# Kernel optimization log

Hardware: AMD Instinct MI355X
Metric: run time of the kernel (lower is better)

The kernel has to match this reference:

```python
import jax, jax.numpy as jnp
import numpy as np

DIM = 512
NL = 4
P = 8
B = 4
L = 8192  # byte-level sequence length
LP = L // P  # patch-level sequence length


def _ln(x, g, b, eps=1e-5):
    m = jnp.mean(x, axis=-1, keepdims=True)
    v = jnp.mean((x - m) ** 2, axis=-1, keepdims=True)
    return (x - m) * jax.lax.rsqrt(v + eps) * g + b


def setup_inputs() -> dict:
    key = jax.random.key(0)
    ks = jax.random.split(key, 24)
    s = 0.02
    inp = {
        "bytes_in": jax.random.randint(ks[0], (B, L), 0, 256, dtype=jnp.int32),
        "byte_emb": jax.random.normal(ks[1], (256, DIM), jnp.float32) * s,
        # patch encoder Conv1d(kernel=stride=P): weight laid out [P, D_in, D_out]
        "enc_w": jax.random.normal(ks[2], (P, DIM, DIM), jnp.float32) * s,
        "enc_b": jnp.zeros((DIM,), jnp.float32),
        "hash_proj": jax.random.normal(ks[3], (DIM, DIM), jnp.float32) * s,
        # per-layer stacked params
        "qkv_w": jax.random.normal(ks[4], (NL, DIM, 3 * DIM), jnp.float32) * s,
        "qkv_b": jnp.zeros((NL, 3 * DIM), jnp.float32),
        "gate_w": jax.random.normal(ks[5], (NL, DIM, DIM), jnp.float32) * s,
        "gate_b": jnp.zeros((NL, DIM), jnp.float32),
        "ln1_g": jnp.ones((NL, DIM), jnp.float32),
        "ln1_b": jnp.zeros((NL, DIM), jnp.float32),
        "mlp_w1": jax.random.normal(ks[6], (NL, DIM, 4 * DIM), jnp.float32) * s,
        "mlp_b1": jnp.zeros((NL, 4 * DIM), jnp.float32),
        "mlp_w2": jax.random.normal(ks[7], (NL, 4 * DIM, DIM), jnp.float32) * s,
        "mlp_b2": jnp.zeros((NL, DIM), jnp.float32),
        "ln2_g": jnp.ones((NL, DIM), jnp.float32),
        "ln2_b": jnp.zeros((NL, DIM), jnp.float32),
        # patch decoder ConvTranspose1d(kernel=stride=P): weight [D_in, P, D_out]
        "dec_w": jax.random.normal(ks[8], (DIM, P, DIM), jnp.float32) * s,
        "dec_b": jnp.zeros((DIM,), jnp.float32),
        "head_w": jax.random.normal(ks[9], (DIM, 256), jnp.float32) * s,
        "head_b": jnp.zeros((256,), jnp.float32),
    }
    return inp


def reference(bytes_in, byte_emb, enc_w, enc_b, hash_proj,
              qkv_w, qkv_b, gate_w, gate_b, ln1_g, ln1_b,
              mlp_w1, mlp_b1, mlp_w2, mlp_b2, ln2_g, ln2_b,
              dec_w, dec_b, head_w, head_b):
    # byte embedding: [B, L, D]
    x = byte_emb[bytes_in]
    # non-overlapping Conv1d(kernel=stride=P) == patch-wise contraction
    xp = x.reshape(B, LP, P, DIM)
    x = jnp.einsum('blpd,pdo->blo', xp, enc_w) + enc_b  # [B, LP, D]
    # hash projection
    x = x + jnp.tanh(x @ hash_proj)
    for i in range(NL):
        # LinearLatentKernel
        h = _ln(x, ln1_g[i], ln1_b[i])
        qkv = h @ qkv_w[i] + qkv_b[i]
        q, k, v = jnp.split(qkv, 3, axis=-1)
        kv_state = jnp.cumsum(k * v, axis=1)
        g = jax.nn.sigmoid(h @ gate_w[i] + gate_b[i])
        x = x + q * kv_state * g
        # MLP
        h = _ln(x, ln2_g[i], ln2_b[i])
        h = jax.nn.gelu(h @ mlp_w1[i] + mlp_b1[i], approximate=False)
        x = x + h @ mlp_w2[i] + mlp_b2[i]
    # ConvTranspose1d(kernel=stride=P): each patch expands to P positions
    y = jnp.einsum('bld,dpo->blpo', x, dec_w).reshape(B, L, DIM) + dec_b
    logits = y @ head_w + head_b  # [B, L, 256]
    return logits
```

## Files before the change

kernel.cpp:

```cpp
#include <hip/hip_runtime.h>
#include <hip/hip_bf16.h>
#include <math.h>

#define DIMD 512
#define NLAYER 4
#define PP 8
#define BBATCH 4
#define LBYTES 8192
#define LPATCH 1024
#define MROWS (BBATCH * LPATCH)

#define NCHUNK 64
#define CLEN   16
#define QGS    (4 * DIMD)

typedef __bf16 bf16x8 __attribute__((ext_vector_type(8)));
typedef float f32x4 __attribute__((ext_vector_type(4)));
typedef unsigned short u16x4 __attribute__((ext_vector_type(4)));
typedef unsigned short u16x8 __attribute__((ext_vector_type(8)));

__device__ __forceinline__ unsigned short f2bf(float f) {
    union { float f; unsigned u; } v; v.f = f;
    unsigned r = v.u + 0x7FFFu + ((v.u >> 16) & 1u);
    return (unsigned short)(r >> 16);
}
__device__ __forceinline__ float bf2f(unsigned short u) {
    union { unsigned u; float f; } v; v.u = ((unsigned)u) << 16;
    return v.f;
}

__device__ __forceinline__ void glds16(const unsigned short* g, unsigned short* l) {
    __builtin_amdgcn_global_load_lds((__attribute__((address_space(1))) void*)g,
                                     (__attribute__((address_space(3))) void*)l,
                                     16, 0, 0);
}

template<int TM, int ACT, bool BIAS, bool RES, bool OBF>
__global__ __launch_bounds__(256)
void mfma_gemm(const unsigned short* __restrict__ A, int lda, long aZ,
               const unsigned short* __restrict__ Bt, int ldb, long bZ,
               const float* __restrict__ bias,
               const float* __restrict__ res, int ldr,
               void* __restrict__ Cv, int ldc, long cZ, int K)
{
    constexpr int M_REP = TM / 32;
    __shared__ unsigned short As[TM * 32];
    __shared__ unsigned short Bs[128 * 32];

    const int tid = threadIdx.x;
    const int w = tid >> 6, l = tid & 63;
    const int row0 = blockIdx.x * TM;
    const int col0 = blockIdx.y * 128;
    A  += (size_t)blockIdx.z * aZ;
    Bt += (size_t)blockIdx.z * bZ;
    unsigned short* Cb = (unsigned short*)Cv + (size_t)blockIdx.z * cZ;
    float*          Cf = (float*)Cv          + (size_t)blockIdx.z * cZ;

    const int cA = w * 64 + l;
    const unsigned short* gA0 = A + (size_t)(row0 + (cA >> 2)) * lda + (cA & 3) * 8;
    const unsigned short* gB0 = Bt + (size_t)(col0 + (cA >> 2)) * ldb + (cA & 3) * 8;
    const unsigned short* gB1 = Bt + (size_t)(col0 + 64 + (cA >> 2)) * ldb + (cA & 3) * 8;
    unsigned short* lA0 = &As[w * 512];
    unsigned short* lB0 = &Bs[w * 512];
    unsigned short* lB1 = &Bs[2048 + w * 512];
    const unsigned short* gA1 = nullptr;
    unsigned short* lA1 = nullptr;
    if constexpr (TM == 128) {
        gA1 = A + (size_t)(row0 + 64 + (cA >> 2)) * lda + (cA & 3) * 8;
        lA1 = &As[2048 + w * 512];
    }

    const int wr = (w >> 1) * (TM / 2);
    const int wc = (w & 1) * 64;
    const int lr = l & 15, lk = (l >> 4) * 8;
    const int aBase = (wr + lr) * 32 + lk;
    const int bBase = (wc + lr) * 32 + lk;

    f32x4 acc[M_REP][4] = {};

    for (int k0 = 0; k0 < K; k0 += 32) {
        glds16(gA0, lA0);  gA0 += 32;
        if constexpr (TM == 128) { glds16(gA1, lA1); gA1 += 32; }
        glds16(gB0, lB0);  gB0 += 32;
        glds16(gB1, lB1);  gB1 += 32;
        __syncthreads();
        bf16x8 af[M_REP], bfr[4];
        #pragma unroll
        for (int m = 0; m < M_REP; m++)
            af[m] = *reinterpret_cast<const bf16x8*>(&As[aBase + m * 512]);
        #pragma unroll
        for (int n = 0; n < 4; n++)
            bfr[n] = *reinterpret_cast<const bf16x8*>(&Bs[bBase + n * 512]);
        #pragma unroll
        for (int m = 0; m < M_REP; m++)
            #pragma unroll
            for (int n = 0; n < 4; n++)
                acc[m][n] = __builtin_amdgcn_mfma_f32_16x16x32_bf16(
                    af[m], bfr[n], acc[m][n], 0, 0, 0);
        __syncthreads();
    }

    const int r0 = row0 + wr + (l >> 4) * 4;
    const int c0 = col0 + wc + lr;
    float bv[4] = {0.f, 0.f, 0.f, 0.f};
    if (BIAS) {
        #pragma unroll
        for (int n = 0; n < 4; n++) bv[n] = bias[c0 + n * 16];
    }
    #pragma unroll
    for (int m = 0; m < M_REP; m++) {
        #pragma unroll
        for (int j = 0; j < 4; j++) {
            const int row = r0 + m * 16 + j;
            #pragma unroll
            for (int n = 0; n < 4; n++) {
                float v = acc[m][n][j];
                if (BIAS) v += bv[n];
                if (ACT == 1) v = tanhf(v);
                if (ACT == 2) v = 0.5f * v * (1.f + erff(v * 0.70710678118f));
                if (RES) v += res[(size_t)row * ldr + c0 + n * 16];
                if (OBF) Cb[(size_t)row * ldc + c0 + n * 16] = f2bf(v);
                else     Cf[(size_t)row * ldc + c0 + n * 16] = v;
            }
        }
    }
}

__device__ __forceinline__ void packT_body(float* sm, const float* __restrict__ in,
                                           unsigned short* __restrict__ out,
                                           int K, int N, int bx, int by)
{
    float (*t)[33] = (float(*)[33])sm;
    const int k0 = bx * 32, n0 = by * 32;
    const int tx = threadIdx.x & 31, ty = threadIdx.x >> 5;
    #pragma unroll
    for (int i = 0; i < 4; i++)
        t[ty + i * 8][tx] = in[(size_t)(k0 + ty + i * 8) * N + n0 + tx];
    __syncthreads();
    #pragma unroll
    for (int i = 0; i < 4; i++)
        out[(size_t)(n0 + ty + i * 8) * K + k0 + tx] = f2bf(t[tx][ty + i * 8]);
}

__device__ __forceinline__ void cast_body(const float* __restrict__ in,
                                          unsigned short* __restrict__ out, int blk)
{
    const long i = ((long)blk * 256 + threadIdx.x) * 8;
    float4 a = *(const float4*)(in + i);
    float4 b = *(const float4*)(in + i + 4);
    u16x8 o;
    o[0] = f2bf(a.x); o[1] = f2bf(a.y); o[2] = f2bf(a.z); o[3] = f2bf(a.w);
    o[4] = f2bf(b.x); o[5] = f2bf(b.y); o[6] = f2bf(b.z); o[7] = f2bf(b.w);
    *reinterpret_cast<u16x8*>(out + i) = o;
}

__global__ __launch_bounds__(256)
void megapack(const float* __restrict__ qkv_w, const float* __restrict__ gate_w,
              const float* __restrict__ mlp_w1, const float* __restrict__ mlp_w2,
              const float* __restrict__ hash_proj, const float* __restrict__ head_w,
              const float* __restrict__ enc_w, const float* __restrict__ dec_w,
              const float* __restrict__ byte_emb,
              const float* __restrict__ qkv_b, const float* __restrict__ gate_b,
              unsigned short* __restrict__ wcat, unsigned short* __restrict__ w1T,
              unsigned short* __restrict__ w2T, unsigned short* __restrict__ whashT,
              unsigned short* __restrict__ hwT, unsigned short* __restrict__ encT,
              unsigned short* __restrict__ decb, unsigned short* __restrict__ embB,
              float* __restrict__ cbias)
{
    __shared__ float sm[32 * 33];
    int id = blockIdx.x;
    if (id < 3072) {
        int z = id / 768, r = id % 768;
        packT_body(sm, qkv_w + (size_t)z * 512 * 1536, wcat + (size_t)z * 2048 * 512,
                   512, 1536, r % 16, r / 16);
    } else if (id < 4096) {
        id -= 3072; int z = id / 256, r = id % 256;
        packT_body(sm, gate_w + (size_t)z * 512 * 512,
                   wcat + (size_t)z * 2048 * 512 + (size_t)1536 * 512,
                   512, 512, r % 16, r / 16);
    } else if (id < 8192) {
        id -= 4096; int z = id / 1024, r = id % 1024;
        packT_body(sm, mlp_w1 + (size_t)z * 512 * 2048, w1T + (size_t)z * 2048 * 512,
                   512, 2048, r % 16, r / 16);
    } else if (id < 12288) {
        id -= 8192; int z = id / 1024, r = id % 1024;
        packT_body(sm, mlp_w2 + (size_t)z * 2048 * 512, w2T + (size_t)z * 512 * 2048,
                   2048, 512, r % 64, r / 64);
    } else if (id < 12544) {
        id -= 12288;
        packT_body(sm, hash_proj, whashT, 512, 512, id % 16, id / 16);
    } else if (id < 12672) {
        id -= 12544;
        packT_body(sm, head_w, hwT, 512, 256, id % 16, id / 16);
    } else if (id < 14720) {
        id -= 12672; int z = id / 256, r = id % 256;
        packT_body(sm, enc_w + (size_t)z * 512 * 512, encT + (size_t)z * 512 * 512,
                   512, 512, r % 16, r / 16);
    } else if (id < 15744) {
        cast_body(dec_w, decb, id - 14720);
    } else if (id < 15808) {
        cast_body(byte_emb, embB, id - 15744);
    } else {
        id -= 15808;
        const int i = id >> 3;
        const int n = (id & 7) * 256 + threadIdx.x;
        cbias[i * 2048 + n] = (n < 1536) ? qkv_b[i * 1536 + n] : gate_b[i * 512 + n - 1536];
    }
}

__global__ __launch_bounds__(256)
void ln_kernel(const float* __restrict__ x, const float* __restrict__ g,
               const float* __restrict__ b, unsigned short* __restrict__ h)
{
    const int row = blockIdx.x * 4 + (threadIdx.x >> 6);
    const int lane = threadIdx.x & 63;
    const float* xr = x + (long)row * DIMD;
    float4 v0 = *(const float4*)(xr + lane * 8);
    float4 v1 = *(const float4*)(xr + lane * 8 + 4);
    float xv[8] = {v0.x, v0.y, v0.z, v0.w, v1.x, v1.y, v1.z, v1.w};
    float s = 0.f, q = 0.f;
    #pragma unroll
    for (int j = 0; j < 8; j++) { s += xv[j]; q += xv[j] * xv[j]; }
    #pragma unroll
    for (int off = 1; off < 64; off <<= 1) {
        s += __shfl_xor(s, off);
        q += __shfl_xor(q, off);
    }
    const float mean = s * (1.f / DIMD);
    const float var  = q * (1.f / DIMD) - mean * mean;
    const float rstd = rsqrtf(var + 1e-5f);
    float4 g0 = *(const float4*)(g + lane * 8);
    float4 g1 = *(const float4*)(g + lane * 8 + 4);
    float4 b0 = *(const float4*)(b + lane * 8);
    float4 b1 = *(const float4*)(b + lane * 8 + 4);
    float gv[8] = {g0.x, g0.y, g0.z, g0.w, g1.x, g1.y, g1.z, g1.w};
    float bb[8] = {b0.x, b0.y, b0.z, b0.w, b1.x, b1.y, b1.z, b1.w};
    u16x8 o;
    #pragma unroll
    for (int j = 0; j < 8; j++) o[j] = f2bf((xv[j] - mean) * rstd * gv[j] + bb[j]);
    *reinterpret_cast<u16x8*>(h + (long)row * DIMD + lane * 8) = o;
}

__global__ __launch_bounds__(128)
void embed_kernel(const int* __restrict__ bytes, const float* __restrict__ E,
                  const float* __restrict__ enc_b, float* __restrict__ x0,
                  unsigned short* __restrict__ x0b)
{
    const int patch = blockIdx.x;
    __shared__ int by[PP];
    if (threadIdx.x < PP) by[threadIdx.x] = bytes[patch * PP + threadIdx.x];
    __syncthreads();
    const int o = threadIdx.x * 4;
    float4 acc = *(const float4*)(enc_b + o);
    #pragma unroll
    for (int p = 0; p < PP; p++) {
        float4 e = *(const float4*)(E + ((long)(p * 256 + by[p])) * DIMD + o);
        acc.x += e.x; acc.y += e.y; acc.z += e.z; acc.w += e.w;
    }
    *(float4*)(x0 + (long)patch * DIMD + o) = acc;
    u16x4 ob; ob[0] = f2bf(acc.x); ob[1] = f2bf(acc.y);
    ob[2] = f2bf(acc.z); ob[3] = f2bf(acc.w);
    *reinterpret_cast<u16x4*>(x0b + (long)patch * DIMD + o) = ob;
}

__global__ __launch_bounds__(256)
void scan_partial(const unsigned short* __restrict__ qg, float* __restrict__ S)
{
    const int b = blockIdx.x >> 6, c = blockIdx.x & 63, d2 = threadIdx.x * 2;
    const unsigned short* base = qg + (size_t)(b * LPATCH + c * CLEN) * QGS;
    float s0 = 0.f, s1 = 0.f;
    for (int l = 0; l < CLEN; l++) {
        ushort2 kk = *(const ushort2*)(base + l * QGS + DIMD + d2);
        ushort2 vv = *(const ushort2*)(base + l * QGS + 2 * DIMD + d2);
        s0 = fmaf(bf2f(kk.x), bf2f(vv.x), s0);
        s1 = fmaf(bf2f(kk.y), bf2f(vv.y), s1);
    }
    *(float2*)(S + (size_t)(b * NCHUNK + c) * DIMD + d2) = make_float2(s0, s1);
}

__global__ __launch_bounds__(512)
void scan_prefix(float* __restrict__ S)
{
    const int b = blockIdx.x, d = threadIdx.x;
    float run = 0.f;
    #pragma unroll 4
    for (int c = 0; c < NCHUNK; c++) {
        float v = S[(b * NCHUNK + c) * DIMD + d];
        S[(b * NCHUNK + c) * DIMD + d] = run;
        run += v;
    }
}

__global__ __launch_bounds__(256)
void scan_apply(const unsigned short* __restrict__ qg,
                const float* __restrict__ S, float* __restrict__ x)
{
    const int b = blockIdx.x >> 6, c = blockIdx.x & 63, d2 = threadIdx.x * 2;
    float2 kv = *(const float2*)(S + (size_t)(b * NCHUNK + c) * DIMD + d2);
    const int row0 = b * LPATCH + c * CLEN;
    for (int l = 0; l < CLEN; l++) {
        const unsigned short* qb = qg + (size_t)(row0 + l) * QGS;
        ushort2 qq = *(const ushort2*)(qb + d2);
        ushort2 kk = *(const ushort2*)(qb + DIMD + d2);
        ushort2 vv = *(const ushort2*)(qb + 2 * DIMD + d2);
        ushort2 gg = *(const ushort2*)(qb + 3 * DIMD + d2);
        kv.x = fmaf(bf2f(kk.x), bf2f(vv.x), kv.x);
        kv.y = fmaf(bf2f(kk.y), bf2f(vv.y), kv.y);
        const float sg0 = 1.f / (1.f + expf(-bf2f(gg.x)));
        const float sg1 = 1.f / (1.f + expf(-bf2f(gg.y)));
        float* xr = x + (size_t)(row0 + l) * DIMD;
        float2 xv = *(const float2*)(xr + d2);
        xv.x += bf2f(qq.x) * kv.x * sg0;
        xv.y += bf2f(qq.y) * kv.y * sg1;
        *(float2*)(xr + d2) = xv;
    }
}

__global__ __launch_bounds__(256)
void fbias2(const unsigned short* __restrict__ hwT, const float* __restrict__ dec_b,
            const float* __restrict__ head_b, float* __restrict__ fb)
{
    const int w = threadIdx.x >> 6, l = threadIdx.x & 63;
    const int o = blockIdx.x * 4 + w;
    u16x8 hv = *reinterpret_cast<const u16x8*>(hwT + (size_t)o * DIMD + l * 8);
    float4 d0 = *(const float4*)(dec_b + l * 8);
    float4 d1 = *(const float4*)(dec_b + l * 8 + 4);
    float dd[8] = {d0.x, d0.y, d0.z, d0.w, d1.x, d1.y, d1.z, d1.w};
    float s = 0.f;
    #pragma unroll
    for (int j = 0; j < 8; j++) s += bf2f(hv[j]) * dd[j];
    #pragma unroll
    for (int off = 1; off < 64; off <<= 1) s += __shfl_xor(s, off);
    if (l == 0) {
        float v = s + head_b[o];
        #pragma unroll
        for (int p = 0; p < PP; p++) fb[p * 256 + o] = v;
    }
}

extern "C" void kernel_launch(void* const* d_in, const int* in_sizes, int n_in,
                              void* d_out, int out_size, void* d_ws, size_t ws_size,
                              hipStream_t stream)
{
    (void)in_sizes; (void)n_in; (void)out_size; (void)ws_size;

    const int*   bytes_in  = (const int*)d_in[0];
    const float* byte_emb  = (const float*)d_in[1];
    const float* enc_w     = (const float*)d_in[2];
    const float* enc_b     = (const float*)d_in[3];
    const float* hash_proj = (const float*)d_in[4];
    const float* qkv_w     = (const float*)d_in[5];
    const float* qkv_b     = (const float*)d_in[6];
    const float* gate_w    = (const float*)d_in[7];
    const float* gate_b    = (const float*)d_in[8];
    const float* ln1_g     = (const float*)d_in[9];
    const float* ln1_b     = (const float*)d_in[10];
    const float* mlp_w1    = (const float*)d_in[11];
    const float* mlp_b1    = (const float*)d_in[12];
    const float* mlp_w2    = (const float*)d_in[13];
    const float* mlp_b2    = (const float*)d_in[14];
    const float* ln2_g     = (const float*)d_in[15];
    const float* ln2_b     = (const float*)d_in[16];
    const float* dec_w     = (const float*)d_in[17];
    const float* dec_b     = (const float*)d_in[18];
    const float* head_w    = (const float*)d_in[19];
    const float* head_b    = (const float*)d_in[20];
    float* out = (float*)d_out;

    char* ws = (char*)d_ws;
    size_t o = 0;
    auto alloc = [&](size_t bytes) { char* p = ws + o; o += (bytes + 255) & ~(size_t)255; return p; };
    unsigned short* wcat   = (unsigned short*)alloc((size_t)4 * 2048 * 512 * 2);
    unsigned short* w1T    = (unsigned short*)alloc((size_t)4 * 2048 * 512 * 2);
    unsigned short* w2T    = (unsigned short*)alloc((size_t)4 * 512 * 2048 * 2);
    unsigned short* whashT = (unsigned short*)alloc((size_t)512 * 512 * 2);
    unsigned short* wWfT   = (unsigned short*)alloc((size_t)2048 * 512 * 2);
    unsigned short* encT   = (unsigned short*)alloc((size_t)8 * 512 * 512 * 2);
    unsigned short* hwT    = (unsigned short*)alloc((size_t)256 * 512 * 2);
    unsigned short* decb   = (unsigned short*)alloc((size_t)512 * 8 * 512 * 2);
    unsigned short* embB   = (unsigned short*)alloc((size_t)256 * 512 * 2);
    float* cbias           = (float*)alloc((size_t)4 * 2048 * 4);
    float* fb              = (float*)alloc(2048 * 4);
    float* E               = (float*)alloc((size_t)8 * 256 * 512 * 4);
    float* x               = (float*)alloc((size_t)MROWS * DIMD * 4);
    float* x0              = (float*)alloc((size_t)MROWS * DIMD * 4);
    unsigned short* x0b    = (unsigned short*)alloc((size_t)MROWS * DIMD * 2);
    unsigned short* h      = (unsigned short*)alloc((size_t)MROWS * DIMD * 2);
    unsigned short* xb     = (unsigned short*)alloc((size_t)MROWS * DIMD * 2);
    float* S               = (float*)alloc((size_t)BBATCH * NCHUNK * DIMD * 4);
    unsigned short* qg     = (unsigned short*)alloc((size_t)MROWS * 2048 * 2);
    unsigned short* hid    = (unsigned short*)alloc((size_t)MROWS * 2048 * 2);

    megapack<<<dim3(15840), 256, 0, stream>>>(
        qkv_w, gate_w, mlp_w1, mlp_w2, hash_proj, head_w, enc_w, dec_w, byte_emb,
        qkv_b, gate_b,
        wcat, w1T, w2T, whashT, hwT, encT, decb, embB, cbias);

    mfma_gemm<64, 0, false, false, true><<<dim3(4, 4, 8), 256, 0, stream>>>(
        hwT, 512, 0L, decb, PP * 512, 512L,
        nullptr, nullptr, 0, wWfT, 512, (long)256 * 512, 512);
    fbias2<<<dim3(64), 256, 0, stream>>>(hwT, dec_b, head_b, fb);

    mfma_gemm<64, 0, false, false, false><<<dim3(4, 4, 8), 256, 0, stream>>>(
        embB, 512, 0L, encT, 512, (long)512 * 512,
        nullptr, nullptr, 0, E, 512, (long)256 * 512, 512);

    embed_kernel<<<dim3(MROWS), dim3(128), 0, stream>>>(bytes_in, E, enc_b, x0, x0b);

    mfma_gemm<64, 1, false, true, false><<<dim3(MROWS / 64, 4, 1), 256, 0, stream>>>(
        x0b, DIMD, 0L, whashT, DIMD, 0L, nullptr, x0, DIMD, x, DIMD, 0L, DIMD);

    for (int i = 0; i < NLAYER; i++) {
        ln_kernel<<<dim3(MROWS / 4), 256, 0, stream>>>(x, ln1_g + i * DIMD, ln1_b + i * DIMD, h);
        mfma_gemm<128, 0, true, false, true><<<dim3(MROWS / 128, 16, 1), 256, 0, stream>>>(
            h, DIMD, 0L, wcat + (size_t)i * 2048 * 512, DIMD, 0L,
            cbias + (size_t)i * 2048, nullptr, 0, qg, 2048, 0L, DIMD);
        scan_partial<<<dim3(BBATCH * NCHUNK), 256, 0, stream>>>(qg, S);
        scan_prefix<<<dim3(BBATCH), dim3(512), 0, stream>>>(S);
        scan_apply<<<dim3(BBATCH * NCHUNK), 256, 0, stream>>>(qg, S, x);
        ln_kernel<<<dim3(MROWS / 4), 256, 0, stream>>>(x, ln2_g + i * DIMD, ln2_b + i * DIMD, h);
        mfma_gemm<128, 2, true, false, true><<<dim3(MROWS / 128, 16, 1), 256, 0, stream>>>(
            h, DIMD, 0L, w1T + (size_t)i * 2048 * 512, DIMD, 0L,
            mlp_b1 + (size_t)i * 2048, nullptr, 0, hid, 2048, 0L, DIMD);
        if (i < NLAYER - 1) {
            mfma_gemm<64, 0, true, true, false><<<dim3(MROWS / 64, 4, 1), 256, 0, stream>>>(
                hid, 2048, 0L, w2T + (size_t)i * 512 * 2048, 2048, 0L,
                mlp_b2 + (size_t)i * DIMD, x, DIMD, x, DIMD, 0L, 2048);
        } else {
            mfma_gemm<64, 0, true, true, true><<<dim3(MROWS / 64, 4, 1), 256, 0, stream>>>(
                hid, 2048, 0L, w2T + (size_t)i * 512 * 2048, 2048, 0L,
                mlp_b2 + (size_t)i * DIMD, x, DIMD, xb, DIMD, 0L, 2048);
        }
    }

    mfma_gemm<128, 0, true, false, false><<<dim3(MROWS / 128, 16, 1), 256, 0, stream>>>(
        xb, DIMD, 0L, wWfT, DIMD, 0L, fb, nullptr, 0, out, 2048, 0L, DIMD);
}
```

Measured before the change: 479.5 us.

## Fuse chunk-sum of k*v into QKV GEMM epilogue via interleaved column layout

Permutes the packed QKV+gate weight columns so each 64-column group holds matching q,k,v,gate slices of 16 dims. The QKV GEMM epilogue can then compute per-16-row chunk sums of k*v directly and write them to S. This removes the scan_partial and scan_prefix kernels; scan_apply now sums the preceding chunk partials itself, which is redundant O(c) work per block. The fbias kernel is also folded into the pack kernel as a single serial block, and bias and weight layouts are remapped to match.

Result: slower. 503.6 us (+5.0%).

```diff
diff --git a/kernel.cpp b/kernel.cpp
--- a/kernel.cpp
+++ b/kernel.cpp
@@ -35,13 +35,14 @@
                                      16, 0, 0);
 }
 
-template<int TM, int ACT, bool BIAS, bool RES, bool OBF>
+template<int TM, int ACT, bool BIAS, bool RES, bool OBF, bool SCAN = false>
 __global__ __launch_bounds__(256)
 void mfma_gemm(const unsigned short* __restrict__ A, int lda, long aZ,
                const unsigned short* __restrict__ Bt, int ldb, long bZ,
                const float* __restrict__ bias,
                const float* __restrict__ res, int ldr,
-               void* __restrict__ Cv, int ldc, long cZ, int K)
+               void* __restrict__ Cv, int ldc, long cZ, int K,
+               float* __restrict__ Sout)
 {
     constexpr int M_REP = TM / 32;
     __shared__ unsigned short As[TM * 32];
@@ -109,26 +110,55 @@
     }
     #pragma unroll
     for (int m = 0; m < M_REP; m++) {
+        float vals[4][4];
+        #pragma unroll
+        for (int n = 0; n < 4; n++)
+            #pragma unroll
+            for (int j = 0; j < 4; j++) {
+                float v = acc[m][n][j];
+                if (BIAS) v += bv[n];
+                if (ACT == 1) v = tanhf(v);
+                if (ACT == 2) v = 0.5f * v * (1.f + erff(v * 0.70710678118f));
+                vals[n][j] = v;
+            }
         #pragma unroll
         for (int j = 0; j < 4; j++) {
             const int row = r0 + m * 16 + j;
             #pragma unroll
             for (int n = 0; n < 4; n++) {
-                float v = acc[m][n][j];
-                if (BIAS) v += bv[n];
-                if (ACT == 1) v = tanhf(v);
-                if (ACT == 2) v = 0.5f * v * (1.f + erff(v * 0.70710678118f));
+                float v = vals[n][j];
                 if (RES) v += res[(size_t)row * ldr + c0 + n * 16];
                 if (OBF) Cb[(size_t)row * ldc + c0 + n * 16] = f2bf(v);
                 else     Cf[(size_t)row * ldc + c0 + n * 16] = v;
             }
         }
-    }
+        if constexpr (SCAN) {
+            float s = 0.f;
+            #pragma unroll
+            for (int j = 0; j < 4; j++) s += vals[1][j] * vals[2][j];
+            s += __shfl_xor(s, 16);
+            s += __shfl_xor(s, 32);
+            if (l < 16) {
+                const int grow = row0 + wr + m * 16;
+                const int sb = grow >> 10, sc = (grow & 1023) >> 4;
+                const int tg = (col0 + wc) >> 6;
+                Sout[(size_t)((sb << 6) + sc) * DIMD + tg * 16 + l] = s;
+            }
+        }
+    }
+}
+
+__device__ __forceinline__ int permcol(int n, int mode) {
+    if (mode == 0) return n;
+    int tau, d;
+    if (mode == 1) { tau = n >> 9; d = n & 511; }
+    else           { tau = 3;      d = n; }
+    return ((d >> 4) << 6) + (tau << 4) + (d & 15);
 }
 
 __device__ __forceinline__ void packT_body(float* sm, const float* __restrict__ in,
                                            unsigned short* __restrict__ out,
-                                           int K, int N, int bx, int by)
+                                           int K, int N, int bx, int by, int mode)
 {
     float (*t)[33] = (float(*)[33])sm;
     const int k0 = bx * 32, n0 = by * 32;
@@ -139,7 +169,7 @@
     __syncthreads();
     #pragma unroll
     for (int i = 0; i < 4; i++)
-        out[(size_t)(n0 + ty + i * 8) * K + k0 + tx] = f2bf(t[tx][ty + i * 8]);
+        out[(size_t)permcol(n0 + ty + i * 8, mode) * K + k0 + tx] = f2bf(t[tx][ty + i * 8]);
 }
 
 __device__ __forceinline__ void cast_body(const float* __restrict__ in,
@@ -161,50 +191,60 @@
               const float* __restrict__ enc_w, const float* __restrict__ dec_w,
               const float* __restrict__ byte_emb,
               const float* __restrict__ qkv_b, const float* __restrict__ gate_b,
+              const float* __restrict__ dec_b, const float* __restrict__ head_b,
               unsigned short* __restrict__ wcat, unsigned short* __restrict__ w1T,
               unsigned short* __restrict__ w2T, unsigned short* __restrict__ whashT,
               unsigned short* __restrict__ hwT, unsigned short* __restrict__ encT,
               unsigned short* __restrict__ decb, unsigned short* __restrict__ embB,
-              float* __restrict__ cbias)
+              float* __restrict__ cbias, float* __restrict__ fb)
 {
     __shared__ float sm[32 * 33];
     int id = blockIdx.x;
     if (id < 3072) {
         int z = id / 768, r = id % 768;
         packT_body(sm, qkv_w + (size_t)z * 512 * 1536, wcat + (size_t)z * 2048 * 512,
-                   512, 1536, r % 16, r / 16);
+                   512, 1536, r % 16, r / 16, 1);
     } else if (id < 4096) {
         id -= 3072; int z = id / 256, r = id % 256;
         packT_body(sm, gate_w + (size_t)z * 512 * 512,
-                   wcat + (size_t)z * 2048 * 512 + (size_t)1536 * 512,
-                   512, 512, r % 16, r / 16);
+                   wcat + (size_t)z * 2048 * 512,
+                   512, 512, r % 16, r / 16, 2);
     } else if (id < 8192) {
         id -= 4096; int z = id / 1024, r = id % 1024;
         packT_body(sm, mlp_w1 + (size_t)z * 512 * 2048, w1T + (size_t)z * 2048 * 512,
-                   512, 2048, r % 16, r / 16);
+                   512, 2048, r % 16, r / 16, 0);
     } else if (id < 12288) {
         id -= 8192; int z = id / 1024, r = id % 1024;
         packT_body(sm, mlp_w2 + (size_t)z * 2048 * 512, w2T + (size_t)z * 512 * 2048,
-                   2048, 512, r % 64, r / 64);
+                   2048, 512, r % 64, r / 64, 0);
     } else if (id < 12544) {
         id -= 12288;
-        packT_body(sm, hash_proj, whashT, 512, 512, id % 16, id / 16);
+        packT_body(sm, hash_proj, whashT, 512, 512, id % 16, id / 16, 0);
     } else if (id < 12672) {
         id -= 12544;
-        packT_body(sm, head_w, hwT, 512, 256, id % 16, id / 16);
+        packT_body(sm, head_w, hwT, 512, 256, id % 16, id / 16, 0);
     } else if (id < 14720) {
         id -= 12672; int z = id / 256, r = id % 256;
         packT_body(sm, enc_w + (size_t)z * 512 * 512, encT + (size_t)z * 512 * 512,
-                   512, 512, r % 16, r / 16);
+                   512, 512, r % 16, r / 16, 0);
     } else if (id < 15744) {
         cast_body(dec_w, decb, id - 14720);
     } else if (id < 15808) {
         cast_body(byte_emb, embB, id - 15744);
-    } else {
+    } else if (id < 15840) {
         id -= 15808;
         const int i = id >> 3;
         const int n = (id & 7) * 256 + threadIdx.x;
-        cbias[i * 2048 + n] = (n < 1536) ? qkv_b[i * 1536 + n] : gate_b[i * 512 + n - 1536];
+        const int t = n >> 6, tau = (n >> 4) & 3, r = n & 15;
+        const int d = t * 16 + r;
+        cbias[i * 2048 + n] = (tau < 3) ? qkv_b[i * 1536 + tau * 512 + d]
+                                        : gate_b[i * 512 + d];
+    } else {
+        const int o = threadIdx.x;
+        float s = head_b[o];
+        for (int d = 0; d < DIMD; d++) s = fmaf(dec_b[d], head_w[d * 256 + o], s);
+        #pragma unroll
+        for (int p = 0; p < PP; p++) fb[p * 256 + o] = s;
     }
 }
 
@@ -264,46 +304,25 @@
 }
 
 __global__ __launch_bounds__(256)
-void scan_partial(const unsigned short* __restrict__ qg, float* __restrict__ S)
-{
-    const int b = blockIdx.x >> 6, c = blockIdx.x & 63, d2 = threadIdx.x * 2;
-    const unsigned short* base = qg + (size_t)(b * LPATCH + c * CLEN) * QGS;
-    float s0 = 0.f, s1 = 0.f;
-    for (int l = 0; l < CLEN; l++) {
-        ushort2 kk = *(const ushort2*)(base + l * QGS + DIMD + d2);
-        ushort2 vv = *(const ushort2*)(base + l * QGS + 2 * DIMD + d2);
-        s0 = fmaf(bf2f(kk.x), bf2f(vv.x), s0);
-        s1 = fmaf(bf2f(kk.y), bf2f(vv.y), s1);
-    }
-    *(float2*)(S + (size_t)(b * NCHUNK + c) * DIMD + d2) = make_float2(s0, s1);
-}
-
-__global__ __launch_bounds__(512)
-void scan_prefix(float* __restrict__ S)
-{
-    const int b = blockIdx.x, d = threadIdx.x;
-    float run = 0.f;
-    #pragma unroll 4
-    for (int c = 0; c < NCHUNK; c++) {
-        float v = S[(b * NCHUNK + c) * DIMD + d];
-        S[(b * NCHUNK + c) * DIMD + d] = run;
-        run += v;
-    }
-}
-
-__global__ __launch_bounds__(256)
 void scan_apply(const unsigned short* __restrict__ qg,
                 const float* __restrict__ S, float* __restrict__ x)
 {
-    const int b = blockIdx.x >> 6, c = blockIdx.x & 63, d2 = threadIdx.x * 2;
-    float2 kv = *(const float2*)(S + (size_t)(b * NCHUNK + c) * DIMD + d2);
+    const int b = blockIdx.x >> 6, c = blockIdx.x & 63;
+    const int d2 = threadIdx.x * 2;
+    const int colq = ((d2 >> 4) << 6) + (d2 & 15);
+    float2 kv = make_float2(0.f, 0.f);
+    const float* Sb = S + (size_t)b * NCHUNK * DIMD + d2;
+    for (int j = 0; j < c; j++) {
+        float2 sv = *(const float2*)(Sb + (size_t)j * DIMD);
+        kv.x += sv.x; kv.y += sv.y;
+    }
     const int row0 = b * LPATCH + c * CLEN;
     for (int l = 0; l < CLEN; l++) {
-        const unsigned short* qb = qg + (size_t)(row0 + l) * QGS;
-        ushort2 qq = *(const ushort2*)(qb + d2);
-        ushort2 kk = *(const ushort2*)(qb + DIMD + d2);
-        ushort2 vv = *(const ushort2*)(qb + 2 * DIMD + d2);
-        ushort2 gg = *(const ushort2*)(qb + 3 * DIMD + d2);
+        const unsigned short* qb = qg + (size_t)(row0 + l) * QGS + colq;
+        ushort2 qq = *(const ushort2*)(qb);
+        ushort2 kk = *(const ushort2*)(qb + 16);
+        ushort2 vv = *(const ushort2*)(qb + 32);
+        ushort2 gg = *(const ushort2*)(qb + 48);
         kv.x = fmaf(bf2f(kk.x), bf2f(vv.x), kv.x);
         kv.y = fmaf(bf2f(kk.y), bf2f(vv.y), kv.y);
         const float sg0 = 1.f / (1.f + expf(-bf2f(gg.x)));
@@ -313,28 +332,6 @@
         xv.x += bf2f(qq.x) * kv.x * sg0;
         xv.y += bf2f(qq.y) * kv.y * sg1;
         *(float2*)(xr + d2) = xv;
-    }
-}
-
-__global__ __launch_bounds__(256)
-void fbias2(const unsigned short* __restrict__ hwT, const float* __restrict__ dec_b,
-            const float* __restrict__ head_b, float* __restrict__ fb)
-{
-    const int w = threadIdx.x >> 6, l = threadIdx.x & 63;
-    const int o = blockIdx.x * 4 + w;
-    u16x8 hv = *reinterpret_cast<const u16x8*>(hwT + (size_t)o * DIMD + l * 8);
-    float4 d0 = *(const float4*)(dec_b + l * 8);
-    float4 d1 = *(const float4*)(dec_b + l * 8 + 4);
-    float dd[8] = {d0.x, d0.y, d0.z, d0.w, d1.x, d1.y, d1.z, d1.w};
-    float s = 0.f;
-    #pragma unroll
-    for (int j = 0; j < 8; j++) s += bf2f(hv[j]) * dd[j];
-    #pragma unroll
-    for (int off = 1; off < 64; off <<= 1) s += __shfl_xor(s, off);
-    if (l == 0) {
-        float v = s + head_b[o];
-        #pragma unroll
-        for (int p = 0; p < PP; p++) fb[p * 256 + o] = v;
     }
 }
 
@@ -391,48 +388,45 @@
     unsigned short* qg     = (unsigned short*)alloc((size_t)MROWS * 2048 * 2);
     unsigned short* hid    = (unsigned short*)alloc((size_t)MROWS * 2048 * 2);
 
-    megapack<<<dim3(15840), 256, 0, stream>>>(
+    megapack<<<dim3(15841), 256, 0, stream>>>(
         qkv_w, gate_w, mlp_w1, mlp_w2, hash_proj, head_w, enc_w, dec_w, byte_emb,
-        qkv_b, gate_b,
-        wcat, w1T, w2T, whashT, hwT, encT, decb, embB, cbias);
+        qkv_b, gate_b, dec_b, head_b,
+        wcat, w1T, w2T, whashT, hwT, encT, decb, embB, cbias, fb);
 
     mfma_gemm<64, 0, false, false, true><<<dim3(4, 4, 8), 256, 0, stream>>>(
         hwT, 512, 0L, decb, PP * 512, 512L,
-        nullptr, nullptr, 0, wWfT, 512, (long)256 * 512, 512);
-    fbias2<<<dim3(64), 256, 0, stream>>>(hwT, dec_b, head_b, fb);
+        nullptr, nullptr, 0, wWfT, 512, (long)256 * 512, 512, nullptr);
 
     mfma_gemm<64, 0, false, false, false><<<dim3(4, 4, 8), 256, 0, stream>>>(
         embB, 512, 0L, encT, 512, (long)512 * 512,
-        nullptr, nullptr, 0, E, 512, (long)256 * 512, 512);
+        nullptr, nullptr, 0, E, 512, (long)256 * 512, 512, nullptr);
 
     embed_kernel<<<dim3(MROWS), dim3(128), 0, stream>>>(bytes_in, E, enc_b, x0, x0b);
 
     mfma_gemm<64, 1, false, true, false><<<dim3(MROWS / 64, 4, 1), 256, 0, stream>>>(
-        x0b, DIMD, 0L, whashT, DIMD, 0L, nullptr, x0, DIMD, x, DIMD, 0L, DIMD);
+        x0b, DIMD, 0L, whashT, DIMD, 0L, nullptr, x0, DIMD, x, DIMD, 0L, DIMD, nullptr);
 
     for (int i = 0; i < NLAYER; i++) {
         ln_kernel<<<dim3(MROWS / 4), 256, 0, stream>>>(x, ln1_g + i * DIMD, ln1_b + i * DIMD, h);
-        mfma_gemm<128, 0, true, false, true><<<dim3(MROWS / 128, 16, 1), 256, 0, stream>>>(
+        mfma_gemm<128, 0, true, false, true, true><<<dim3(MROWS / 128, 16, 1), 256, 0, stream>>>(
             h, DIMD, 0L, wcat + (size_t)i * 2048 * 512, DIMD, 0L,
-            cbias + (size_t)i * 2048, nullptr, 0, qg, 2048, 0L, DIMD);
-        scan_partial<<<dim3(BBATCH * NCHUNK), 256, 0, stream>>>(qg, S);
-        scan_prefix<<<dim3(BBATCH), dim3(512), 0, stream>>>(S);
+            cbias + (size_t)i * 2048, nullptr, 0, qg, 2048, 0L, DIMD, S);
         scan_apply<<<dim3(BBATCH * NCHUNK), 256, 0, stream>>>(qg, S, x);
         ln_kernel<<<dim3(MROWS / 4), 256, 0, stream>>>(x, ln2_g + i * DIMD, ln2_b + i * DIMD, h);
         mfma_gemm<128, 2, true, false, true><<<dim3(MROWS / 128, 16, 1), 256, 0, stream>>>(
             h, DIMD, 0L, w1T + (size_t)i * 2048 * 512, DIMD, 0L,
-            mlp_b1 + (size_t)i * 2048, nullptr, 0, hid, 2048, 0L, DIMD);
+            mlp_b1 + (size_t)i * 2048, nullptr, 0, hid, 2048, 0L, DIMD, nullptr);
         if (i < NLAYER - 1) {
             mfma_gemm<64, 0, true, true, false><<<dim3(MROWS / 64, 4, 1), 256, 0, stream>>>(
                 hid, 2048, 0L, w2T + (size_t)i * 512 * 2048, 2048, 0L,
-                mlp_b2 + (size_t)i * DIMD, x, DIMD, x, DIMD, 0L, 2048);
+                mlp_b2 + (size_t)i * DIMD, x, DIMD, x, DIMD, 0L, 2048, nullptr);
         } else {
             mfma_gemm<64, 0, true, true, true><<<dim3(MROWS / 64, 4, 1), 256, 0, stream>>>(
                 hid, 2048, 0L, w2T + (size_t)i * 512 * 2048, 2048, 0L,
-                mlp_b2 + (size_t)i * DIMD, x, DIMD, xb, DIMD, 0L, 2048);
+                mlp_b2 + (size_t)i * DIMD, x, DIMD, xb, DIMD, 0L, 2048, nullptr);
         }
     }
 
     mfma_gemm<128, 0, true, false, false><<<dim3(MROWS / 128, 16, 1), 256, 0, stream>>>(
-        xb, DIMD, 0L, wWfT, DIMD, 0L, fb, nullptr, 0, out, 2048, 0L, DIMD);
-}
+        xb, DIMD, 0L, wWfT, DIMD, 0L, fb, nullptr, 0, out, 2048, 0L, DIMD, nullptr);
+}
```
